# Kernel tuning notes

Measured on AMD Instinct MI355X. Metric: run time of the kernel, lower is better.

Reference implementation:

```python
import jax, jax.numpy as jnp
import numpy as np

LATENT_CH = 1024
INPUT_CH = 768
QK_CH = 1024
V_CH = 1024
OUT_CH = 1024
NHEADS = 8
EPS = 1e-5


def layer_norm(x, gamma, beta):
    mu = jnp.mean(x, axis=-1, keepdims=True)
    var = jnp.var(x, axis=-1, keepdims=True)
    return (x - mu) * jax.lax.rsqrt(var + EPS) * gamma + beta


def setup_inputs() -> dict:
    key = jax.random.key(0)
    ks = jax.random.split(key, 6)
    B, Lq, Lkv = 8, 512, 16384
    latent_q = jax.random.normal(ks[0], (B, Lq, LATENT_CH), dtype=jnp.float32)
    input_kv = jax.random.normal(ks[1], (B, Lkv, INPUT_CH), dtype=jnp.float32)
    # weights stored [in, out] so projection is x @ W
    W_Q = jax.random.normal(ks[2], (LATENT_CH, QK_CH), dtype=jnp.float32) / np.sqrt(LATENT_CH)
    W_K = jax.random.normal(ks[3], (INPUT_CH, QK_CH), dtype=jnp.float32) / np.sqrt(INPUT_CH)
    W_V = jax.random.normal(ks[4], (INPUT_CH, V_CH), dtype=jnp.float32) / np.sqrt(INPUT_CH)
    W_O = jax.random.normal(ks[5], (V_CH, OUT_CH), dtype=jnp.float32) / np.sqrt(V_CH)
    ln_lat_g = jnp.ones((LATENT_CH,), jnp.float32)
    ln_lat_b = jnp.zeros((LATENT_CH,), jnp.float32)
    ln_in_g = jnp.ones((INPUT_CH,), jnp.float32)
    ln_in_b = jnp.zeros((INPUT_CH,), jnp.float32)
    return dict(latent_q=latent_q, input_kv=input_kv, W_Q=W_Q, W_K=W_K, W_V=W_V, W_O=W_O,
                ln_lat_g=ln_lat_g, ln_lat_b=ln_lat_b, ln_in_g=ln_in_g, ln_in_b=ln_in_b)


def reference(latent_q, input_kv, W_Q, W_K, W_V, W_O, ln_lat_g, ln_lat_b, ln_in_g, ln_in_b):
    B, Lq, _ = latent_q.shape
    _, Lkv, _ = input_kv.shape
    H = NHEADS
    dqk = QK_CH // H
    dv = V_CH // H

    lat = layer_norm(latent_q, ln_lat_g, ln_lat_b)
    inp = layer_norm(input_kv, ln_in_g, ln_in_b)

    Q = (lat @ W_Q).reshape(B, Lq, H, dqk)   # [B, Lq, H, dqk]
    K = (inp @ W_K).reshape(B, Lkv, H, dqk)  # [B, Lkv, H, dqk]
    V = (inp @ W_V).reshape(B, Lkv, H, dv)   # [B, Lkv, H, dv]

    scale = 1.0 / np.sqrt(dqk).astype(np.float32)
    attn = jnp.einsum('bqhd,bkhd->bhqk', Q, K) * scale
    attn = jax.nn.softmax(attn, axis=-1)
    # dropout is identity at eval / p used deterministically here
    out = jnp.einsum('bhqk,bkhd->bqhd', attn, V).reshape(B, Lq, V_CH)
    return out @ W_O
```

## Files before the change

### kernel.cpp

```cpp
#include <hip/hip_runtime.h>


typedef __bf16 bf16x8 __attribute__((ext_vector_type(8)));
typedef float f32x4 __attribute__((ext_vector_type(4)));
typedef unsigned short us4 __attribute__((ext_vector_type(4)));
typedef unsigned int u32;
typedef unsigned short u16;

#define MFMA_BF16(a, b, c) __builtin_amdgcn_mfma_f32_16x16x32_bf16(a, b, c, 0, 0, 0)

__device__ __forceinline__ u16 f2b(float f) {
    u32 x = __builtin_bit_cast(u32, f);
    x += 0x7fffu + ((x >> 16) & 1u);
    return (u16)(x >> 16);
}

typedef const __attribute__((address_space(1))) unsigned int gl_u32;
typedef __attribute__((address_space(3))) unsigned int lds_u32;

__device__ __forceinline__ void g2l16(const u16* g, u16* l) {
    __builtin_amdgcn_global_load_lds((gl_u32*)g, (lds_u32*)l, 16, 0, 0);
}

__global__ void transpose_f32_bf16(const float* __restrict__ in,
                                   u16* __restrict__ out, int R, int C) {
    __shared__ u16 t[32][33];
    int tx = threadIdx.x, ty = threadIdx.y;
    int bx = blockIdx.x * 32, by = blockIdx.y * 32;
#pragma unroll
    for (int j = 0; j < 4; j++)
        t[ty + j * 8][tx] = f2b(in[(long)(by + ty + j * 8) * C + bx + tx]);
    __syncthreads();
#pragma unroll
    for (int j = 0; j < 4; j++)
        out[(long)(bx + ty + j * 8) * R + by + tx] = t[tx][ty + j * 8];
}

__global__ __launch_bounds__(256) void ln_rows(const float* __restrict__ x,
                                               const float* __restrict__ g,
                                               const float* __restrict__ bt,
                                               u16* __restrict__ y, int C) {
    long row = blockIdx.x;
    int tid = threadIdx.x;
    const float4* xf = (const float4*)(x + row * C);
    int C4 = C >> 2;
    float s = 0.f, ss = 0.f;
    for (int i = tid; i < C4; i += 256) {
        float4 v = xf[i];
        s += v.x + v.y + v.z + v.w;
        ss += v.x * v.x + v.y * v.y + v.z * v.z + v.w * v.w;
    }
#pragma unroll
    for (int off = 1; off < 64; off <<= 1) {
        s += __shfl_xor(s, off);
        ss += __shfl_xor(ss, off);
    }
    __shared__ float red[2][4];
    int wave = tid >> 6;
    if ((tid & 63) == 0) { red[0][wave] = s; red[1][wave] = ss; }
    __syncthreads();
    s = red[0][0] + red[0][1] + red[0][2] + red[0][3];
    ss = red[1][0] + red[1][1] + red[1][2] + red[1][3];
    float inv = 1.f / (float)C;
    float mu = s * inv;
    float var = ss * inv - mu * mu;
    float rstd = rsqrtf(var + 1e-5f);
    const float4* gf = (const float4*)g;
    const float4* bf_ = (const float4*)bt;
    for (int i = tid; i < C4; i += 256) {
        float4 v = xf[i], gv = gf[i], bv = bf_[i];
        us4 pk;
        pk[0] = f2b((v.x - mu) * rstd * gv.x + bv.x);
        pk[1] = f2b((v.y - mu) * rstd * gv.y + bv.y);
        pk[2] = f2b((v.z - mu) * rstd * gv.z + bv.z);
        pk[3] = f2b((v.w - mu) * rstd * gv.w + bv.w);
        *(us4*)&y[row * C + i * 4] = pk;
    }
}

template <int VSTORE, int F32OUT>
__global__ __launch_bounds__(256, 2) void gemm_bt(const u16* __restrict__ A,
                                                  const u16* __restrict__ Bt,
                                                  void* __restrict__ Cv, int Kd) {
    __shared__ u16 As[128][32];
    __shared__ u16 Bs[128][32];
    int tid = threadIdx.x;
    int lane = tid & 63, wave = tid >> 6;
    int l15 = lane & 15, quad = lane >> 4;
    int wm = (wave >> 1) << 6, wn = (wave & 1) << 6;
    int bid = blockIdx.x + (blockIdx.y << 3);
    int xcd = bid & 7, j = bid >> 3;
    int n0 = (j & 7) << 7;
    long m0 = (long)(((j >> 3) << 3) + xcd) << 7;
    int r0 = tid >> 2, sg = (tid & 3) << 3;
    const u16* a0 = A + (m0 + r0) * Kd + sg;
    const u16* a1 = a0 + (long)64 * Kd;
    const u16* bp0 = Bt + (long)(n0 + r0) * Kd + sg;
    const u16* bp1 = bp0 + (long)64 * Kd;
    u16* As0 = &As[r0][sg];
    u16* As1 = &As[r0 + 64][sg];
    u16* Bs0 = &Bs[r0][sg];
    u16* Bs1 = &Bs[r0 + 64][sg];
    f32x4 acc[4][4] = {};
    for (int k0 = 0; k0 < Kd; k0 += 32) {
        g2l16(a0 + k0, As0);
        g2l16(a1 + k0, As1);
        g2l16(bp0 + k0, Bs0);
        g2l16(bp1 + k0, Bs1);
        __syncthreads();
        bf16x8 af[4], bf[4];
#pragma unroll
        for (int mt = 0; mt < 4; mt++)
            af[mt] = *(const bf16x8*)&As[wm + mt * 16 + l15][quad * 8];
#pragma unroll
        for (int nt = 0; nt < 4; nt++)
            bf[nt] = *(const bf16x8*)&Bs[wn + nt * 16 + l15][quad * 8];
#pragma unroll
        for (int mt = 0; mt < 4; mt++)
#pragma unroll
            for (int nt = 0; nt < 4; nt++)
                acc[mt][nt] = MFMA_BF16(af[mt], bf[nt], acc[mt][nt]);
        __syncthreads();
    }
#pragma unroll
    for (int mt = 0; mt < 4; mt++) {
#pragma unroll
        for (int nt = 0; nt < 4; nt++) {
            int col = n0 + wn + nt * 16 + l15;
            long rowb = m0 + wm + mt * 16 + quad * 4;
            if constexpr (VSTORE) {
                u16* C = (u16*)Cv;
                int bl = (int)(rowb >> 14);
                int key = (int)(rowb & 16383);
                us4 pk;
#pragma unroll
                for (int r = 0; r < 4; r++) pk[r] = f2b(acc[mt][nt][r]);
                *(us4*)&C[((long)(bl * 1024 + col) << 14) + key] = pk;
            } else if constexpr (F32OUT) {
                float* C = (float*)Cv;
#pragma unroll
                for (int r = 0; r < 4; r++)
                    C[(rowb + r) * 1024 + col] = acc[mt][nt][r];
            } else {
                u16* C = (u16*)Cv;
#pragma unroll
                for (int r = 0; r < 4; r++)
                    C[(rowb + r) * 1024 + col] = f2b(acc[mt][nt][r]);
            }
        }
    }
}

__global__ __launch_bounds__(512, 2) void attn_fwd(const u16* __restrict__ Qb,
                                                   const u16* __restrict__ Kb,
                                                   const u16* __restrict__ Vt,
                                                   float* __restrict__ Opart,
                                                   float* __restrict__ Ml, int b0) {
    int h = blockIdx.x & 7, bl = blockIdx.x >> 3;
    int qtile = blockIdx.y >> 1, half = blockIdx.y & 1;
    int rows = gridDim.x << 6;
    int tid = threadIdx.x, lane = tid & 63, wave = tid >> 6;
    int l15 = lane & 15, quad = lane >> 4;
    int l7 = l15 & 7;

    __shared__ __align__(16) char smem[98304];
    u16* KB = (u16*)smem;
    u16* VB = (u16*)(smem + 32768);
    u16* Pw = (u16*)(smem + 65536) + wave * 2048;
    u16(*Qs)[136] = (u16(*)[136])smem;

    long qrow0 = (long)(b0 + bl) * 512 + qtile * 256;
#pragma unroll
    for (int i = 0; i < 8; i++) {
        int L = tid + i * 512;
        int row = L >> 4, seg = L & 15;
        *(uint4*)&Qs[row][seg * 8] =
            *(const uint4*)&Qb[(qrow0 + row) * 1024 + h * 128 + seg * 8];
    }
    __syncthreads();
    bf16x8 qf[2][4];
#pragma unroll
    for (int nt = 0; nt < 2; nt++)
#pragma unroll
        for (int kc = 0; kc < 4; kc++)
            qf[nt][kc] = *(const bf16x8*)&Qs[wave * 32 + nt * 16 + l15][kc * 32 + quad * 8];
    __syncthreads();

    const u16* Kg = Kb + ((long)bl * 16384 + half * 8192) * 1024 + h * 128;
    const u16* Vg = Vt + ((long)(bl * 1024 + h * 128)) * 16384 + half * 8192;

    int S0 = tid, S1 = tid + 512;
    int kO0 = (S0 >> 4) * 1024 + (((S0 & 15) ^ ((S0 >> 4) & 7)) << 3);
    int kO1 = (S1 >> 4) * 1024 + (((S1 & 15) ^ ((S1 >> 4) & 7)) << 3);
    long vO0 = (long)(S0 >> 3) * 16384 + (((S0 & 7) ^ ((S0 >> 3) & 7)) << 3);
    long vO1 = (long)(S1 >> 3) * 16384 + (((S1 & 7) ^ ((S1 >> 3) & 7)) << 3);

    g2l16(Kg + kO0, KB + S0 * 8);
    g2l16(Kg + kO1, KB + S1 * 8);
    g2l16(Vg + vO0, VB + S0 * 8);
    g2l16(Vg + vO1, VB + S1 * 8);
    __syncthreads();

    f32x4 o[2][8] = {};
    float m_run[2] = {-1e30f, -1e30f};
    float l_run[2] = {0.f, 0.f};
    const float scl = 0.08838834764831845f;

    int cur = 0;
    for (int it = 0; it < 128; it++) {
        const u16* Kc = KB + cur * 8192;
        const u16* Vc = VB + cur * 8192;
        if (it < 127) {
            long kb = (long)(it + 1) << 16;
            int vb = (it + 1) << 6;
            u16* Kn = KB + (cur ^ 1) * 8192;
            u16* Vn = VB + (cur ^ 1) * 8192;
            g2l16(Kg + kb + kO0, Kn + S0 * 8);
            g2l16(Kg + kb + kO1, Kn + S1 * 8);
            g2l16(Vg + vb + vO0, Vn + S0 * 8);
            g2l16(Vg + vb + vO1, Vn + S1 * 8);
        }

        f32x4 s[4][2] = {};
#pragma unroll
        for (int kc = 0; kc < 4; kc++) {
            int ks = (((kc << 2) + quad) ^ l7) << 3;
            bf16x8 kf[4];
#pragma unroll
            for (int mt = 0; mt < 4; mt++)
                kf[mt] = *(const bf16x8*)&Kc[(mt * 16 + l15) * 128 + ks];
#pragma unroll
            for (int mt = 0; mt < 4; mt++) {
                s[mt][0] = MFMA_BF16(kf[mt], qf[0][kc], s[mt][0]);
                s[mt][1] = MFMA_BF16(kf[mt], qf[1][kc], s[mt][1]);
            }
        }

#pragma unroll
        for (int nt = 0; nt < 2; nt++) {
            float pm = -1e30f;
#pragma unroll
            for (int mt = 0; mt < 4; mt++)
#pragma unroll
                for (int r = 0; r < 4; r++) pm = fmaxf(pm, s[mt][nt][r]);
            pm = fmaxf(pm, __shfl_xor(pm, 16));
            pm = fmaxf(pm, __shfl_xor(pm, 32));
            float mnew = fmaxf(m_run[nt], pm);
            float alpha = __expf((m_run[nt] - mnew) * scl);
            m_run[nt] = mnew;
            float mc = mnew * scl;
            float psum = 0.f;
            int pbase = (nt * 16 + l15) * 64 + ((quad & 1) << 2);
#pragma unroll
            for (int mt = 0; mt < 4; mt++) {
                us4 pk;
#pragma unroll
                for (int r = 0; r < 4; r++) {
                    float p = __expf(s[mt][nt][r] * scl - mc);
                    psum += p;
                    pk[r] = f2b(p);
                }
                *(us4*)&Pw[pbase + ((((mt << 1) + (quad >> 1)) ^ l7) << 3)] = pk;
            }
            psum += __shfl_xor(psum, 16);
            psum += __shfl_xor(psum, 32);
            l_run[nt] = l_run[nt] * alpha + psum;
            float af_[4];
#pragma unroll
            for (int r = 0; r < 4; r++) af_[r] = __shfl(alpha, quad * 4 + r);
#pragma unroll
            for (int n = 0; n < 8; n++)
#pragma unroll
                for (int r = 0; r < 4; r++) o[nt][n][r] *= af_[r];
        }

#pragma unroll
        for (int kc = 0; kc < 2; kc++) {
            int sl = (((kc << 2) + quad) ^ l7) << 3;
            bf16x8 pf0 = *(const bf16x8*)&Pw[l15 * 64 + sl];
            bf16x8 pf1 = *(const bf16x8*)&Pw[(16 + l15) * 64 + sl];
#pragma unroll
            for (int n = 0; n < 8; n++) {
                bf16x8 vf = *(const bf16x8*)&Vc[(n * 16 + l15) * 64 + sl];
                o[0][n] = MFMA_BF16(pf0, vf, o[0][n]);
                o[1][n] = MFMA_BF16(pf1, vf, o[1][n]);
            }
        }
        __syncthreads();
        cur ^= 1;
    }

    long prq = (long)bl * 512 + qtile * 256 + wave * 32;
    float* Oh = Opart + ((long)half * rows) * 1024 + h * 128;
#pragma unroll
    for (int nt = 0; nt < 2; nt++) {
        if (quad == 0) {
            long qi = (long)half * rows + prq + nt * 16 + l15;
            Ml[(qi * 8 + h) * 2] = m_run[nt];
            Ml[(qi * 8 + h) * 2 + 1] = l_run[nt];
        }
#pragma unroll
        for (int n = 0; n < 8; n++)
#pragma unroll
            for (int r = 0; r < 4; r++)
                Oh[(prq + nt * 16 + quad * 4 + r) * 1024 + n * 16 + l15] = o[nt][n][r];
    }
}

__global__ __launch_bounds__(256) void attn_merge(const float* __restrict__ Op,
                                                  const float* __restrict__ Ml,
                                                  u16* __restrict__ Ob, int b0,
                                                  int rows) {
    int pr = blockIdx.x, tid = threadIdx.x;
    const float scl = 0.08838834764831845f;
    long b0r = (long)(b0 * 512 + pr) * 1024;
    long p0 = (long)pr * 1024, p1 = ((long)rows + pr) * 1024;
#pragma unroll
    for (int rep = 0; rep < 4; rep++) {
        int col = tid + rep * 256;
        int h = col >> 7;
        long mi0 = ((long)pr * 8 + h) * 2;
        long mi1 = (((long)rows + pr) * 8 + h) * 2;
        float m0 = Ml[mi0], l0 = Ml[mi0 + 1];
        float m1 = Ml[mi1], l1 = Ml[mi1 + 1];
        float M = fmaxf(m0, m1);
        float a0 = __expf((m0 - M) * scl), a1 = __expf((m1 - M) * scl);
        float v = (Op[p0 + col] * a0 + Op[p1 + col] * a1) / (l0 * a0 + l1 * a1);
        Ob[b0r + col] = f2b(v);
    }
}

extern "C" void kernel_launch(void* const* d_in, const int* in_sizes, int n_in,
                              void* d_out, int out_size, void* d_ws, size_t ws_size,
                              hipStream_t stream) {
    const float* latent = (const float*)d_in[0];
    const float* inpkv = (const float*)d_in[1];
    const float* W_Q = (const float*)d_in[2];
    const float* W_K = (const float*)d_in[3];
    const float* W_V = (const float*)d_in[4];
    const float* W_O = (const float*)d_in[5];
    const float* g_lat = (const float*)d_in[6];
    const float* b_lat = (const float*)d_in[7];
    const float* g_in = (const float*)d_in[8];
    const float* b_in = (const float*)d_in[9];
    float* out = (float*)d_out;

    u16* ws = (u16*)d_ws;
    u16* WtQ = ws;  ws += 1024L * 1024;
    u16* WtK = ws;  ws += 1024L * 768;
    u16* WtV = ws;  ws += 1024L * 768;
    u16* WtO = ws;  ws += 1024L * 1024;
    u16* Aq = ws;   ws += 4096L * 1024;
    u16* Qbuf = ws; ws += 4096L * 1024;
    u16* Obuf = ws; ws += 4096L * 1024;
    size_t fixed_bytes = (size_t)((char*)ws - (char*)d_ws);
    size_t per_batch = (size_t)(16384L * 768 + 2 * 16384L * 1024) * 2;
    int bstep = 1;
    for (int b = 8; b >= 1; b >>= 1)
        if (ws_size >= fixed_bytes + (size_t)b * per_batch) { bstep = b; break; }
    u16* Akv = ws;
    u16* Kbf = Akv + (long)bstep * 16384 * 768;
    u16* Vtb = Kbf + (long)bstep * 16384 * 1024;
    int rows = bstep * 512;
    float* Opart = (float*)Akv;
    float* Mlp = Opart + (long)2 * rows * 1024;

    dim3 t328(32, 8);
    transpose_f32_bf16<<<dim3(32, 32), t328, 0, stream>>>(W_Q, WtQ, 1024, 1024);
    transpose_f32_bf16<<<dim3(32, 24), t328, 0, stream>>>(W_K, WtK, 768, 1024);
    transpose_f32_bf16<<<dim3(32, 24), t328, 0, stream>>>(W_V, WtV, 768, 1024);
    transpose_f32_bf16<<<dim3(32, 32), t328, 0, stream>>>(W_O, WtO, 1024, 1024);

    ln_rows<<<4096, 256, 0, stream>>>(latent, g_lat, b_lat, Aq, 1024);
    gemm_bt<0, 0><<<dim3(8, 32), 256, 0, stream>>>(Aq, WtQ, Qbuf, 1024);

    for (int b0 = 0; b0 < 8; b0 += bstep) {
        ln_rows<<<bstep * 16384, 256, 0, stream>>>(inpkv + (long)b0 * 16384 * 768,
                                                   g_in, b_in, Akv, 768);
        gemm_bt<0, 0><<<dim3(8, bstep * 128), 256, 0, stream>>>(Akv, WtK, Kbf, 768);
        gemm_bt<1, 0><<<dim3(8, bstep * 128), 256, 0, stream>>>(Akv, WtV, Vtb, 768);
        attn_fwd<<<dim3(bstep * 8, 4), 512, 0, stream>>>(Qbuf, Kbf, Vtb, Opart, Mlp, b0);
        attn_merge<<<rows, 256, 0, stream>>>(Opart, Mlp, Obuf, b0, rows);
    }
    gemm_bt<0, 1><<<dim3(8, 32), 256, 0, stream>>>(Obuf, WtO, out, 1024);
}
```

Measured before the change: 1.575 ms.

## Double-buffer GEMM LDS tiles and add lazy softmax rescaling with exp2

The GEMM kernel now keeps two LDS buffers so the next K-slice is loaded while the MFMAs run on the current one, which hides global-load latency. The attention kernel switches to exp2 with a pre-folded log2e scale. It only rescales the running output and sum when the row max grows by more than a threshold, which skips most alpha multiplies on the 8x16 accumulators. It also raises wave priority around the MFMA blocks. The lazy rescale allows unnormalised probabilities up to about 2^8 before the max is refreshed. That could cost bf16 precision of P, and the threshold is in raw-score units rather than scaled units.

```diff
diff --git a/kernel.cpp b/kernel.cpp
--- a/kernel.cpp
+++ b/kernel.cpp
@@ -82,8 +82,8 @@
 __global__ __launch_bounds__(256, 2) void gemm_bt(const u16* __restrict__ A,
                                                   const u16* __restrict__ Bt,
                                                   void* __restrict__ Cv, int Kd) {
-    __shared__ u16 As[128][32];
-    __shared__ u16 Bs[128][32];
+    __shared__ u16 As[2][128][32];
+    __shared__ u16 Bs[2][128][32];
     int tid = threadIdx.x;
     int lane = tid & 63, wave = tid >> 6;
     int l15 = lane & 15, quad = lane >> 4;
@@ -97,31 +97,40 @@
     const u16* a1 = a0 + (long)64 * Kd;
     const u16* bp0 = Bt + (long)(n0 + r0) * Kd + sg;
     const u16* bp1 = bp0 + (long)64 * Kd;
-    u16* As0 = &As[r0][sg];
-    u16* As1 = &As[r0 + 64][sg];
-    u16* Bs0 = &Bs[r0][sg];
-    u16* Bs1 = &Bs[r0 + 64][sg];
     f32x4 acc[4][4] = {};
-    for (int k0 = 0; k0 < Kd; k0 += 32) {
-        g2l16(a0 + k0, As0);
-        g2l16(a1 + k0, As1);
-        g2l16(bp0 + k0, Bs0);
-        g2l16(bp1 + k0, Bs1);
+
+#define STAGE(B, KO)                                \
+    do {                                            \
+        g2l16(a0 + (KO), &As[B][r0][sg]);           \
+        g2l16(a1 + (KO), &As[B][r0 + 64][sg]);      \
+        g2l16(bp0 + (KO), &Bs[B][r0][sg]);          \
+        g2l16(bp1 + (KO), &Bs[B][r0 + 64][sg]);     \
+    } while (0)
+
+#define COMPUTE(B)                                                             \
+    do {                                                                       \
+        bf16x8 af[4], bf[4];                                                   \
+        _Pragma("unroll") for (int mt = 0; mt < 4; mt++)                       \
+            af[mt] = *(const bf16x8*)&As[B][wm + mt * 16 + l15][quad * 8];     \
+        _Pragma("unroll") for (int nt = 0; nt < 4; nt++)                       \
+            bf[nt] = *(const bf16x8*)&Bs[B][wn + nt * 16 + l15][quad * 8];     \
+        _Pragma("unroll") for (int mt = 0; mt < 4; mt++)                       \
+            _Pragma("unroll") for (int nt = 0; nt < 4; nt++)                   \
+                acc[mt][nt] = MFMA_BF16(af[mt], bf[nt], acc[mt][nt]);          \
+    } while (0)
+
+    STAGE(0, 0);
+    __syncthreads();
+    for (int k0 = 0; k0 < Kd; k0 += 64) {
+        STAGE(1, k0 + 32);
+        COMPUTE(0);
         __syncthreads();
-        bf16x8 af[4], bf[4];
-#pragma unroll
-        for (int mt = 0; mt < 4; mt++)
-            af[mt] = *(const bf16x8*)&As[wm + mt * 16 + l15][quad * 8];
-#pragma unroll
-        for (int nt = 0; nt < 4; nt++)
-            bf[nt] = *(const bf16x8*)&Bs[wn + nt * 16 + l15][quad * 8];
-#pragma unroll
-        for (int mt = 0; mt < 4; mt++)
-#pragma unroll
-            for (int nt = 0; nt < 4; nt++)
-                acc[mt][nt] = MFMA_BF16(af[mt], bf[nt], acc[mt][nt]);
+        if (k0 + 64 < Kd) STAGE(0, k0 + 64);
+        COMPUTE(1);
         __syncthreads();
     }
+#undef STAGE
+#undef COMPUTE
 #pragma unroll
     for (int mt = 0; mt < 4; mt++) {
 #pragma unroll
@@ -204,7 +213,7 @@
     f32x4 o[2][8] = {};
     float m_run[2] = {-1e30f, -1e30f};
     float l_run[2] = {0.f, 0.f};
-    const float scl = 0.08838834764831845f;
+    const float scl2 = 0.12751542f;
 
     int cur = 0;
     for (int it = 0; it < 128; it++) {
@@ -222,6 +231,7 @@
         }
 
         f32x4 s[4][2] = {};
+        __builtin_amdgcn_s_setprio(1);
 #pragma unroll
         for (int kc = 0; kc < 4; kc++) {
             int ks = (((kc << 2) + quad) ^ l7) << 3;
@@ -235,6 +245,7 @@
                 s[mt][1] = MFMA_BF16(kf[mt], qf[1][kc], s[mt][1]);
             }
         }
+        __builtin_amdgcn_s_setprio(0);
 
 #pragma unroll
         for (int nt = 0; nt < 2; nt++) {
@@ -245,10 +256,20 @@
                 for (int r = 0; r < 4; r++) pm = fmaxf(pm, s[mt][nt][r]);
             pm = fmaxf(pm, __shfl_xor(pm, 16));
             pm = fmaxf(pm, __shfl_xor(pm, 32));
-            float mnew = fmaxf(m_run[nt], pm);
-            float alpha = __expf((m_run[nt] - mnew) * scl);
-            m_run[nt] = mnew;
-            float mc = mnew * scl;
+            if (__any(pm > m_run[nt] + 64.f)) {
+                float mnew = fmaxf(m_run[nt], pm);
+                float alpha = exp2f((m_run[nt] - mnew) * scl2);
+                m_run[nt] = mnew;
+                l_run[nt] *= alpha;
+                float af_[4];
+#pragma unroll
+                for (int r = 0; r < 4; r++) af_[r] = __shfl(alpha, quad * 4 + r);
+#pragma unroll
+                for (int n = 0; n < 8; n++)
+#pragma unroll
+                    for (int r = 0; r < 4; r++) o[nt][n][r] *= af_[r];
+            }
+            float mc = m_run[nt] * scl2;
             float psum = 0.f;
             int pbase = (nt * 16 + l15) * 64 + ((quad & 1) << 2);
 #pragma unroll
@@ -256,7 +277,7 @@
                 us4 pk;
 #pragma unroll
                 for (int r = 0; r < 4; r++) {
-                    float p = __expf(s[mt][nt][r] * scl - mc);
+                    float p = exp2f(s[mt][nt][r] * scl2 - mc);
                     psum += p;
                     pk[r] = f2b(p);
                 }
@@ -264,16 +285,10 @@
             }
             psum += __shfl_xor(psum, 16);
             psum += __shfl_xor(psum, 32);
-            l_run[nt] = l_run[nt] * alpha + psum;
-            float af_[4];
-#pragma unroll
-            for (int r = 0; r < 4; r++) af_[r] = __shfl(alpha, quad * 4 + r);
-#pragma unroll
-            for (int n = 0; n < 8; n++)
-#pragma unroll
-                for (int r = 0; r < 4; r++) o[nt][n][r] *= af_[r];
-        }
-
+            l_run[nt] += psum;
+        }
+
+        __builtin_amdgcn_s_setprio(1);
 #pragma unroll
         for (int kc = 0; kc < 2; kc++) {
             int sl = (((kc << 2) + quad) ^ l7) << 3;
@@ -286,6 +301,7 @@
                 o[1][n] = MFMA_BF16(pf1, vf, o[1][n]);
             }
         }
+        __builtin_amdgcn_s_setprio(0);
         __syncthreads();
         cur ^= 1;
     }
```

New measurement: 1.620 ms. +2.8%, slower.
